# Optimization experiments

Measured on AMD Instinct MI355X. Metric: run time of the kernel, lower is better.

The kernel has to match this reference:

```python
import jax, jax.numpy as jnp
import numpy as np

NEG_SLOPE = 0.01  # F.leaky_relu default


def grid_sample_bilinear(im, pts):
    """torch.nn.functional.grid_sample equivalent, mode='bilinear',
    align_corners=True, padding_mode='zeros'.
    im: [B, C, H, W], pts: [B, N, 2] in [-1, 1] (x, y order). Returns [B, C, N].
    """
    B, C, H, W = im.shape
    x = (pts[..., 0] + 1.0) * 0.5 * (W - 1)  # [B, N]
    y = (pts[..., 1] + 1.0) * 0.5 * (H - 1)
    x0 = jnp.floor(x)
    y0 = jnp.floor(y)
    wx1 = x - x0
    wy1 = y - y0
    wx0 = 1.0 - wx1
    wy0 = 1.0 - wy1
    x0i = x0.astype(jnp.int32)
    y0i = y0.astype(jnp.int32)
    x1i = x0i + 1
    y1i = y0i + 1

    def corner(yi, xi, w):
        valid = (xi >= 0) & (xi < W) & (yi >= 0) & (yi < H)
        yc = jnp.clip(yi, 0, H - 1)
        xc = jnp.clip(xi, 0, W - 1)
        # gather per-batch: [B, C, N]
        g = jax.vmap(lambda f, yy, xx: f[:, yy, xx])(im, yc, xc)
        return g * (w * valid.astype(im.dtype))[:, None, :]

    return (corner(y0i, x0i, wy0 * wx0) + corner(y0i, x1i, wy0 * wx1)
            + corner(y1i, x0i, wy1 * wx0) + corner(y1i, x1i, wy1 * wx1))


def conv1x1(x, w, b):
    # x: [B, Cin, N], w: [Cout, Cin], b: [Cout] -> [B, Cout, N]
    return jnp.einsum('oi,bin->bon', w, x) + b[None, :, None]


def setup_inputs() -> dict:
    key = jax.random.key(0)
    ks = jax.random.split(key, 9)
    B, N, C, H, W = 64, 6890, 256, 56, 56
    filter_channels = [256, 128, 64, 5]
    points = jax.random.uniform(ks[0], (B, N, 2), jnp.float32, -1.0, 1.0)
    im_feat = jax.random.normal(ks[1], (B, C, H, W), jnp.float32)

    def mk_conv(k, cin, cout):
        k1, k2 = jax.random.split(k)
        bound = 1.0 / np.sqrt(cin)
        w = jax.random.uniform(k1, (cout, cin), jnp.float32, -bound, bound)
        b = jax.random.uniform(k2, (cout,), jnp.float32, -bound, bound)
        return w, b

    w0, b0 = mk_conv(ks[2], filter_channels[0], filter_channels[1])
    w1, b1 = mk_conv(ks[3], filter_channels[1] + filter_channels[0], filter_channels[2])
    w2, b2 = mk_conv(ks[4], filter_channels[2] + filter_channels[0], filter_channels[3])
    return {"points": points, "im_feat": im_feat,
            "w0": w0, "b0": b0, "w1": w1, "b1": b1, "w2": w2, "b2": b2}


def reference(points, im_feat, w0, b0, w1, b1, w2, b2):
    # sampling: bilinear gather of point-wise features, [B, C_s, N]
    point_feat = grid_sample_bilinear(im_feat, points)
    # reduce_dim: 1x1 conv MLP with skip-concat of the input features
    y = jax.nn.leaky_relu(conv1x1(point_feat, w0, b0), NEG_SLOPE)
    y = jax.nn.leaky_relu(conv1x1(jnp.concatenate([y, point_feat], axis=1), w1, b1), NEG_SLOPE)
    y = conv1x1(jnp.concatenate([y, point_feat], axis=1), w2, b2)  # last layer: no leaky_relu
    y = jax.nn.relu(y)  # self.last_op
    mesh_align_feat = y.reshape(y.shape[0], -1)  # [B, C_p * N]
    return (mesh_align_feat, point_feat)
```

## Files before the change

### kernel.cpp

```cpp
#include <hip/hip_runtime.h>

#define B_    64
#define C_    256
#define H_    56
#define W_    56
#define N_    6890
#define HW_   3136
#define NTILE 108

#define WB1_OFF (128*256)
#define WB2_OFF (128*256 + 64*384)
#define WTOT    (128*256 + 64*384 + 5*320)

typedef __attribute__((ext_vector_type(8))) __bf16 bf16x8;
typedef __attribute__((ext_vector_type(8))) unsigned short ushort8;
typedef __attribute__((ext_vector_type(4))) float f32x4;
typedef __attribute__((ext_vector_type(2))) float f32x2;
typedef __attribute__((ext_vector_type(4))) unsigned int uint4v;
typedef __attribute__((ext_vector_type(2))) unsigned int uint2v;

__device__ __forceinline__ unsigned short f2bf(float f) {
    unsigned int u = __builtin_bit_cast(unsigned int, f);
    u += 0x7FFFu + ((u >> 16) & 1u);
    return (unsigned short)(u >> 16);
}
__device__ __forceinline__ unsigned int pack2(float lo, float hi) {
    return (unsigned int)f2bf(lo) | ((unsigned int)f2bf(hi) << 16);
}
__device__ __forceinline__ float leaky(float v) { return v > 0.f ? v : 0.01f * v; }
__device__ __forceinline__ int pswz(int p) { return p ^ ((p >> 3) & 7); }

__global__ void wconv_kernel(const float* __restrict__ w0, const float* __restrict__ w1,
                             const float* __restrict__ w2, unsigned short* __restrict__ wb) {
    int i = blockIdx.x * 256 + threadIdx.x;
    if (i >= WTOT) return;
    float v = (i < WB1_OFF) ? w0[i] : (i < WB2_OFF) ? w1[i - WB1_OFF] : w2[i - WB2_OFF];
    wb[i] = f2bf(v);
}

__global__ __launch_bounds__(512, 6) void gather_kernel(
    const float* __restrict__ points, const float* __restrict__ im,
    float* __restrict__ out1) {
    __shared__ float Ls[HW_ * 4];

    const int t   = threadIdx.x;
    const int bid = blockIdx.x;
    const int b  = ((bid & 7) << 3) | ((bid >> 3) & 7);
    const int ch = bid >> 6;

    const f32x4* im4 = (const f32x4*)(im + ((size_t)b * C_ + ch * 4) * HW_);
#pragma unroll
    for (int g0 = 0; g0 < 2; g0++) {
        int g = t + (g0 << 9);
        if (g < 784) {
            f32x4 r0 = im4[g];
            f32x4 r1 = im4[784 + g];
            f32x4 r2 = im4[1568 + g];
            f32x4 r3 = im4[2352 + g];
#pragma unroll
            for (int i = 0; i < 4; i++) {
                f32x4 v; v[0] = r0[i]; v[1] = r1[i]; v[2] = r2[i]; v[3] = r3[i];
                *(f32x4*)(Ls + (pswz((g << 2) + i) << 2)) = v;
            }
        }
    }
    __syncthreads();

    const float* ptb = points + (size_t)b * N_ * 2;
    const size_t ob0 = ((size_t)b * C_ + ch * 4) * N_;
#pragma unroll 2
    for (int p = 0; p < 14; p++) {
        int n = t + (p << 9);
        if (n < N_) {
            f32x2 pt = *(const f32x2*)(ptb + 2 * n);
            float fx = fminf(fmaxf((pt.x + 1.f) * 27.5f, 0.f), 55.f);
            float fy = fminf(fmaxf((pt.y + 1.f) * 27.5f, 0.f), 55.f);
            float x0f = floorf(fx), y0f = floorf(fy);
            int x0 = (int)x0f, y0 = (int)y0f;
            float wx1 = fx - x0f, wy1 = fy - y0f;
            float wx0 = 1.f - wx1, wy0 = 1.f - wy1;
            bool hix = x0 >= W_ - 1;
            int   xb  = hix ? W_ - 2 : x0;
            float wxl = hix ? 0.f : wx0;
            float wxr = hix ? wx0 : wx1;
            int y0c = min(y0, H_ - 1);
            int y1c = min(y0 + 1, H_ - 1);
            float w00 = wy0 * wxl, w01 = wy0 * wxr;
            float w10 = wy1 * wxl, w11 = wy1 * wxr;
            int ia0 = y0c * W_ + xb, ia1 = y1c * W_ + xb;

            f32x4 q00 = *(const f32x4*)(Ls + (pswz(ia0)     << 2));
            f32x4 q01 = *(const f32x4*)(Ls + (pswz(ia0 + 1) << 2));
            f32x4 q10 = *(const f32x4*)(Ls + (pswz(ia1)     << 2));
            f32x4 q11 = *(const f32x4*)(Ls + (pswz(ia1 + 1) << 2));
            float v0 = w00*q00[0] + w01*q01[0] + w10*q10[0] + w11*q11[0];
            float v1 = w00*q00[1] + w01*q01[1] + w10*q10[1] + w11*q11[1];
            float v2 = w00*q00[2] + w01*q01[2] + w10*q10[2] + w11*q11[2];
            float v3 = w00*q00[3] + w01*q01[3] + w10*q10[3] + w11*q11[3];
            out1[ob0 + n]          = v0;
            out1[ob0 + N_ + n]     = v1;
            out1[ob0 + 2*N_ + n]   = v2;
            out1[ob0 + 3*N_ + n]   = v3;
        }
    }
}

__device__ __forceinline__ bf16x8 afrag_f32(const float* __restrict__ wp, int ldk,
                                            int rowbase, int k0, int lane, int nrows) {
    int i = rowbase + (lane & 15);
    int k = k0 + ((lane >> 4) << 3);
    ushort8 u;
    if (i < nrows) {
        const float* s = wp + (size_t)i * ldk + k;
#pragma unroll
        for (int j = 0; j < 8; j++) u[j] = f2bf(s[j]);
    } else {
#pragma unroll
        for (int j = 0; j < 8; j++) u[j] = 0;
    }
    return __builtin_bit_cast(bf16x8, u);
}
__device__ __forceinline__ bf16x8 afrag_bf(const unsigned short* __restrict__ wb, int ldk,
                                           int rowbase, int k0, int lane, int nrows) {
    int i = rowbase + (lane & 15);
    int k = k0 + ((lane >> 4) << 3);
    if (i < nrows) return __builtin_bit_cast(bf16x8, *(const ushort8*)(wb + (size_t)i * ldk + k));
    ushort8 z = {0, 0, 0, 0, 0, 0, 0, 0};
    return __builtin_bit_cast(bf16x8, z);
}

__device__ __forceinline__ bf16x8 bfrag(const unsigned int* buf, int rowstride_dw,
                                        int n, int k0) {
    int cd = (k0 >> 1) ^ ((n & 7) << 2);
    uint4v v = *(const uint4v*)(buf + n * rowstride_dw + cd);
    return __builtin_bit_cast(bf16x8, v);
}

template <bool BF16W>
__global__ __launch_bounds__(256) void mlp_kernel(
    const float* __restrict__ pf,
    const float* __restrict__ w0, const float* __restrict__ b0,
    const float* __restrict__ w1, const float* __restrict__ b1,
    const float* __restrict__ w2, const float* __restrict__ b2,
    const unsigned short* __restrict__ wb,
    float* __restrict__ out0) {
    __shared__ unsigned int Xs[64 * 128];
    __shared__ unsigned int Y0s[64 * 64];

    const int t    = threadIdx.x;
    const int lane = t & 63;
    const int wave = t >> 6;
    const int bid  = blockIdx.x;
    const int b    = bid / NTILE;
    const int tile = bid - b * NTILE;
    const int n0   = tile * 64;

    const int nn_g = min(n0 + lane, N_ - 1);
    const int swz  = (lane & 7) << 2;

    const float* pfb = pf + (size_t)b * C_ * N_;
#pragma unroll
    for (int g8 = 0; g8 < 8; g8++) {
        int c0 = wave * 64 + g8 * 8;
        float v[8];
#pragma unroll
        for (int j = 0; j < 8; j++) v[j] = pfb[(size_t)(c0 + j) * N_ + nn_g];
        uint4v pk;
        pk[0] = pack2(v[0], v[1]); pk[1] = pack2(v[2], v[3]);
        pk[2] = pack2(v[4], v[5]); pk[3] = pack2(v[6], v[7]);
        *(uint4v*)(Xs + lane * 128 + ((c0 >> 1) ^ swz)) = pk;
    }

    bf16x8 a1[2][8];
#pragma unroll
    for (int mt = 0; mt < 2; mt++)
#pragma unroll
        for (int ks = 0; ks < 8; ks++)
            a1[mt][ks] = BF16W ? afrag_bf(wb, 256, (wave * 2 + mt) * 16, ks * 32, lane, 1 << 30)
                               : afrag_f32(w0, 256, (wave * 2 + mt) * 16, ks * 32, lane, 1 << 30);

    __syncthreads();

    const int cl = lane & 15;
    const int rh = lane >> 4;
    const int kq = rh << 3;

    f32x4 acc1[2][4] = {};
#pragma unroll
    for (int ks = 0; ks < 8; ks++) {
        bf16x8 bx[4];
#pragma unroll
        for (int nt = 0; nt < 4; nt++)
            bx[nt] = bfrag(Xs, 128, nt * 16 + cl, ks * 32 + kq);
#pragma unroll
        for (int mt = 0; mt < 2; mt++)
#pragma unroll
            for (int nt = 0; nt < 4; nt++)
                acc1[mt][nt] = __builtin_amdgcn_mfma_f32_16x16x32_bf16(
                    a1[mt][ks], bx[nt], acc1[mt][nt], 0, 0, 0);
    }

#pragma unroll
    for (int mt = 0; mt < 2; mt++) {
        int m0 = (wave * 2 + mt) * 16 + (rh << 2);
        f32x4 bias = *(const f32x4*)(b0 + m0);
#pragma unroll
        for (int nt = 0; nt < 4; nt++) {
            int nn = nt * 16 + cl;
            float v0 = leaky(acc1[mt][nt][0] + bias[0]);
            float v1 = leaky(acc1[mt][nt][1] + bias[1]);
            float v2 = leaky(acc1[mt][nt][2] + bias[2]);
            float v3 = leaky(acc1[mt][nt][3] + bias[3]);
            int md = (m0 >> 1) ^ ((nn & 7) << 2);
            uint2v pk; pk[0] = pack2(v0, v1); pk[1] = pack2(v2, v3);
            *(uint2v*)(Y0s + nn * 64 + md) = pk;
        }
    }

    bf16x8 a2[12];
#pragma unroll
    for (int ks = 0; ks < 12; ks++)
        a2[ks] = BF16W ? afrag_bf(wb + WB1_OFF, 384, wave * 16, ks * 32, lane, 1 << 30)
                       : afrag_f32(w1, 384, wave * 16, ks * 32, lane, 1 << 30);

    __syncthreads();

    f32x4 acc2[4] = {};
#pragma unroll
    for (int ks = 0; ks < 12; ks++) {
#pragma unroll
        for (int nt = 0; nt < 4; nt++) {
            bf16x8 bx = (ks < 4) ? bfrag(Y0s, 64, nt * 16 + cl, ks * 32 + kq)
                                 : bfrag(Xs, 128, nt * 16 + cl, (ks - 4) * 32 + kq);
            acc2[nt] = __builtin_amdgcn_mfma_f32_16x16x32_bf16(a2[ks], bx, acc2[nt], 0, 0, 0);
        }
    }

    bf16x8 a3[10];
#pragma unroll
    for (int ks = 0; ks < 10; ks++)
        a3[ks] = BF16W ? afrag_bf(wb + WB2_OFF, 320, 0, ks * 32, lane, 5)
                       : afrag_f32(w2, 320, 0, ks * 32, lane, 5);

    __syncthreads();

    {
        int m0 = wave * 16 + (rh << 2);
        f32x4 bias = *(const f32x4*)(b1 + m0);
#pragma unroll
        for (int nt = 0; nt < 4; nt++) {
            int nn = nt * 16 + cl;
            float v0 = leaky(acc2[nt][0] + bias[0]);
            float v1 = leaky(acc2[nt][1] + bias[1]);
            float v2 = leaky(acc2[nt][2] + bias[2]);
            float v3 = leaky(acc2[nt][3] + bias[3]);
            int md = (m0 >> 1) ^ ((nn & 7) << 2);
            uint2v pk; pk[0] = pack2(v0, v1); pk[1] = pack2(v2, v3);
            *(uint2v*)(Y0s + nn * 32 + md) = pk;
        }
    }

    __syncthreads();

    {
        int nn = wave * 16 + cl;
        f32x4 acc3 = {};
#pragma unroll
        for (int ks = 0; ks < 10; ks++) {
            bf16x8 bx = (ks < 2) ? bfrag(Y0s, 32, nn, ks * 32 + kq)
                                 : bfrag(Xs, 128, nn, (ks - 2) * 32 + kq);
            acc3 = __builtin_amdgcn_mfma_f32_16x16x32_bf16(a3[ks], bx, acc3, 0, 0, 0);
        }
        int gn2 = n0 + nn;
        if (gn2 < N_) {
#pragma unroll
            for (int r = 0; r < 4; r++) {
                int m = (rh << 2) + r;
                if (m < 5) {
                    float v = acc3[r] + b2[m];
                    v = v > 0.f ? v : 0.f;
                    out0[((size_t)b * 5 + m) * N_ + gn2] = v;
                }
            }
        }
    }
}

extern "C" void kernel_launch(void* const* d_in, const int* in_sizes, int n_in,
                              void* d_out, int out_size, void* d_ws, size_t ws_size,
                              hipStream_t stream) {
    const float* points = (const float*)d_in[0];
    const float* im     = (const float*)d_in[1];
    const float* w0     = (const float*)d_in[2];
    const float* b0     = (const float*)d_in[3];
    const float* w1     = (const float*)d_in[4];
    const float* b1     = (const float*)d_in[5];
    const float* w2     = (const float*)d_in[6];
    const float* b2     = (const float*)d_in[7];
    float* out0 = (float*)d_out;
    float* out1 = out0 + (size_t)B_ * 5 * N_;

    const size_t WBYTES = (size_t)WTOT * 2;
    const bool wok = (d_ws != nullptr) && (ws_size >= WBYTES);
    unsigned short* wb = (unsigned short*)d_ws;

    if (wok) {
        hipLaunchKernelGGL(wconv_kernel, dim3((WTOT + 255) / 256), dim3(256), 0, stream,
                           w0, w1, w2, wb);
    }
    hipLaunchKernelGGL(gather_kernel, dim3(B_ * 64), dim3(512), 0, stream,
                       points, im, out1);
    if (wok) {
        hipLaunchKernelGGL(mlp_kernel<true>, dim3(B_ * NTILE), dim3(256), 0, stream,
                           out1, w0, b0, w1, b1, w2, b2, wb, out0);
    } else {
        hipLaunchKernelGGL(mlp_kernel<false>, dim3(B_ * NTILE), dim3(256), 0, stream,
                           out1, w0, b0, w1, b1, w2, b2, (const unsigned short*)nullptr, out0);
    }
}
```

Measured before the change: 318.2 us.

## Split gather and MLP into batch chunks for L2/MALL reuse of point features

Launches the gather and MLP kernels in two chunks of 32 batches each instead of one pass over all 64 batches. Batch indices are remapped so each XCD handles the same batches in both kernels, and the MLP visits batches in reverse order of the gather. The intent is that the point features the gather just wrote are still in the XCD-local L2 or the last-level cache when the MLP reads them, avoiding a full HBM round trip of the large intermediate. The cost is extra kernel launches and smaller grids per launch, which can leave tail gaps between kernels.

```diff
diff --git a/kernel.cpp b/kernel.cpp
--- a/kernel.cpp
+++ b/kernel.cpp
@@ -7,6 +7,7 @@
 #define N_    6890
 #define HW_   3136
 #define NTILE 108
+#define GB_   32
 
 #define WB1_OFF (128*256)
 #define WB2_OFF (128*256 + 64*384)
@@ -40,13 +41,15 @@
 
 __global__ __launch_bounds__(512, 6) void gather_kernel(
     const float* __restrict__ points, const float* __restrict__ im,
-    float* __restrict__ out1) {
+    float* __restrict__ out1, int b0) {
     __shared__ float Ls[HW_ * 4];
 
     const int t   = threadIdx.x;
     const int bid = blockIdx.x;
-    const int b  = ((bid & 7) << 3) | ((bid >> 3) & 7);
-    const int ch = bid >> 6;
+    const int xcd  = bid & 7;
+    const int ch   = (bid >> 3) & 63;
+    const int blow = bid >> 9;
+    const int b    = b0 + (blow << 3) + xcd;
 
     const f32x4* im4 = (const f32x4*)(im + ((size_t)b * C_ + ch * 4) * HW_);
 #pragma unroll
@@ -139,11 +142,11 @@
 template <bool BF16W>
 __global__ __launch_bounds__(256) void mlp_kernel(
     const float* __restrict__ pf,
-    const float* __restrict__ w0, const float* __restrict__ b0,
+    const float* __restrict__ w0, const float* __restrict__ b0_,
     const float* __restrict__ w1, const float* __restrict__ b1,
     const float* __restrict__ w2, const float* __restrict__ b2,
     const unsigned short* __restrict__ wb,
-    float* __restrict__ out0) {
+    float* __restrict__ out0, int b0) {
     __shared__ unsigned int Xs[64 * 128];
     __shared__ unsigned int Y0s[64 * 64];
 
@@ -151,9 +154,12 @@
     const int lane = t & 63;
     const int wave = t >> 6;
     const int bid  = blockIdx.x;
-    const int b    = bid / NTILE;
-    const int tile = bid - b * NTILE;
-    const int n0   = tile * 64;
+    const int xcd   = bid & 7;
+    const int r     = bid >> 3;
+    const int tile  = r % NTILE;
+    const int blowr = (GB_ / 8 - 1) - r / NTILE;
+    const int b     = b0 + (blowr << 3) + xcd;
+    const int n0    = tile * 64;
 
     const int nn_g = min(n0 + lane, N_ - 1);
     const int swz  = (lane & 7) << 2;
@@ -203,7 +209,7 @@
 #pragma unroll
     for (int mt = 0; mt < 2; mt++) {
         int m0 = (wave * 2 + mt) * 16 + (rh << 2);
-        f32x4 bias = *(const f32x4*)(b0 + m0);
+        f32x4 bias = *(const f32x4*)(b0_ + m0);
 #pragma unroll
         for (int nt = 0; nt < 4; nt++) {
             int nn = nt * 16 + cl;
@@ -274,10 +280,10 @@
         int gn2 = n0 + nn;
         if (gn2 < N_) {
 #pragma unroll
-            for (int r = 0; r < 4; r++) {
-                int m = (rh << 2) + r;
+            for (int r2 = 0; r2 < 4; r2++) {
+                int m = (rh << 2) + r2;
                 if (m < 5) {
-                    float v = acc3[r] + b2[m];
+                    float v = acc3[r2] + b2[m];
                     v = v > 0.f ? v : 0.f;
                     out0[((size_t)b * 5 + m) * N_ + gn2] = v;
                 }
@@ -308,13 +314,17 @@
         hipLaunchKernelGGL(wconv_kernel, dim3((WTOT + 255) / 256), dim3(256), 0, stream,
                            w0, w1, w2, wb);
     }
-    hipLaunchKernelGGL(gather_kernel, dim3(B_ * 64), dim3(512), 0, stream,
-                       points, im, out1);
-    if (wok) {
-        hipLaunchKernelGGL(mlp_kernel<true>, dim3(B_ * NTILE), dim3(256), 0, stream,
-                           out1, w0, b0, w1, b1, w2, b2, wb, out0);
-    } else {
-        hipLaunchKernelGGL(mlp_kernel<false>, dim3(B_ * NTILE), dim3(256), 0, stream,
-                           out1, w0, b0, w1, b1, w2, b2, (const unsigned short*)nullptr, out0);
-    }
-}
+    for (int g = 0; g < B_ / GB_; g++) {
+        const int bb = g * GB_;
+        hipLaunchKernelGGL(gather_kernel, dim3(GB_ * 64), dim3(512), 0, stream,
+                           points, im, out1, bb);
+        if (wok) {
+            hipLaunchKernelGGL(mlp_kernel<true>, dim3(GB_ * NTILE), dim3(256), 0, stream,
+                               out1, w0, b0, w1, b1, w2, b2, wb, out0, bb);
+        } else {
+            hipLaunchKernelGGL(mlp_kernel<false>, dim3(GB_ * NTILE), dim3(256), 0, stream,
+                               out1, w0, b0, w1, b1, w2, b2,
+                               (const unsigned short*)nullptr, out0, bb);
+        }
+    }
+}
```

Result: slower. 334.3 us (+5.1%).

## Transpose image to channels-last and fuse bilinear gather into MLP kernel

Applied to the files above, without the earlier changes.

Adds a transpose kernel that converts the image feature map to [B, HW, C] layout in workspace. A new fused kernel then gathers bilinear samples per point directly from global memory as contiguous channel vectors, writes point_feat, and runs the three-layer MFMA MLP from shared memory. This removes the re-read of the full point_feat tensor by the separate MLP kernel. In exchange it adds a full image transpose pass (about 200MB of traffic) and relies on cached global gathers instead of LDS-resident image tiles. It needs a large workspace and otherwise falls back to the old path.

```diff
diff --git a/kernel.cpp b/kernel.cpp
--- a/kernel.cpp
+++ b/kernel.cpp
@@ -38,34 +38,294 @@
     wb[i] = f2bf(v);
 }
 
+__global__ __launch_bounds__(256) void transpose_kernel(
+    const float* __restrict__ im, float* __restrict__ imT) {
+    __shared__ float Lt[64][68];
+    const int t   = threadIdx.x;
+    const int bid = blockIdx.x;
+    const int xcd  = bid & 7;
+    const int rest = bid >> 3;
+    const int b    = ((rest & 7) << 3) + xcd;
+    const int tl   = rest >> 3;
+    const int pt   = tl % 49, ct = tl / 49;
+    const int p0   = pt * 64, c0 = ct * 64;
+
+    const float* src = im + ((size_t)b * C_ + c0) * HW_ + p0;
+#pragma unroll
+    for (int rr = 0; rr < 4; rr++) {
+        int c_loc = (t >> 4) + rr * 16;
+        int pq    = (t & 15) << 2;
+        f32x4 v = *(const f32x4*)(src + (size_t)c_loc * HW_ + pq);
+        Lt[c_loc][pq]     = v[0];
+        Lt[c_loc][pq + 1] = v[1];
+        Lt[c_loc][pq + 2] = v[2];
+        Lt[c_loc][pq + 3] = v[3];
+    }
+    __syncthreads();
+    float* dst = imT + ((size_t)b * HW_ + p0) * C_ + c0;
+#pragma unroll
+    for (int i = 0; i < 4; i++) {
+        int idx = t + (i << 8);
+        int pr  = idx >> 4;
+        int c4  = (idx & 15) << 2;
+        f32x4 v;
+        v[0] = Lt[c4][pr]; v[1] = Lt[c4 + 1][pr];
+        v[2] = Lt[c4 + 2][pr]; v[3] = Lt[c4 + 3][pr];
+        *(f32x4*)(dst + (size_t)pr * C_ + c4) = v;
+    }
+}
+
+__device__ __forceinline__ bf16x8 bfrag(const unsigned int* buf, int rowstride_dw,
+                                        int n, int k0) {
+    int cd = (k0 >> 1) ^ ((n & 7) << 2);
+    uint4v v = *(const uint4v*)(buf + n * rowstride_dw + cd);
+    return __builtin_bit_cast(bf16x8, v);
+}
+__device__ __forceinline__ bf16x8 afrag_bf(const unsigned short* __restrict__ wb, int ldk,
+                                           int rowbase, int k0, int lane, int nrows) {
+    int i = rowbase + (lane & 15);
+    int k = k0 + ((lane >> 4) << 3);
+    if (i < nrows) return __builtin_bit_cast(bf16x8, *(const ushort8*)(wb + (size_t)i * ldk + k));
+    ushort8 z = {0, 0, 0, 0, 0, 0, 0, 0};
+    return __builtin_bit_cast(bf16x8, z);
+}
+
+__global__ __launch_bounds__(256, 2) void fused_kernel(
+    const float* __restrict__ points, const float* __restrict__ imT,
+    const float* __restrict__ b0_, const float* __restrict__ b1,
+    const float* __restrict__ b2, const unsigned short* __restrict__ wb,
+    float* __restrict__ out0, float* __restrict__ out1) {
+    __shared__ float Ls[16384];
+    __shared__ float Pw[64][4];
+    __shared__ int   Pi[64][2];
+
+    const int t    = threadIdx.x;
+    const int lane = t & 63;
+    const int wave = t >> 6;
+    const int bid  = blockIdx.x;
+    const int xcd  = bid & 7;
+    const int rr   = bid >> 3;
+    const int tile = rr % NTILE;
+    const int b    = (rr / NTILE) * 8 + xcd;
+    const int n0   = tile * 64;
+
+    if (t < 64) {
+        int n = min(n0 + t, N_ - 1);
+        f32x2 pt = *(const f32x2*)(points + ((size_t)b * N_ + n) * 2);
+        float fx = fminf(fmaxf((pt.x + 1.f) * 27.5f, 0.f), 55.f);
+        float fy = fminf(fmaxf((pt.y + 1.f) * 27.5f, 0.f), 55.f);
+        float x0f = floorf(fx), y0f = floorf(fy);
+        int x0 = (int)x0f, y0 = (int)y0f;
+        float wx1 = fx - x0f, wy1 = fy - y0f;
+        float wx0 = 1.f - wx1, wy0 = 1.f - wy1;
+        bool hix = x0 >= W_ - 1;
+        int   xb  = hix ? W_ - 2 : x0;
+        float wxl = hix ? 0.f : wx0;
+        float wxr = hix ? wx0 : wx1;
+        int y0c = min(y0, H_ - 1);
+        int y1c = min(y0 + 1, H_ - 1);
+        Pw[t][0] = wy0 * wxl; Pw[t][1] = wy0 * wxr;
+        Pw[t][2] = wy1 * wxl; Pw[t][3] = wy1 * wxr;
+        Pi[t][0] = y0c * W_ + xb; Pi[t][1] = y1c * W_ + xb;
+    }
+    __syncthreads();
+
+    const float* ib = imT + (size_t)b * HW_ * C_;
+#pragma unroll
+    for (int i = 0; i < 16; i += 2) {
+        int pA = wave * 16 + i, pB = pA + 1;
+        float wA0 = Pw[pA][0], wA1 = Pw[pA][1], wA2 = Pw[pA][2], wA3 = Pw[pA][3];
+        float wB0 = Pw[pB][0], wB1 = Pw[pB][1], wB2 = Pw[pB][2], wB3 = Pw[pB][3];
+        int aA0 = Pi[pA][0], aA1 = Pi[pA][1];
+        int aB0 = Pi[pB][0], aB1 = Pi[pB][1];
+        const float* sA0 = ib + ((size_t)aA0 << 8) + (lane << 2);
+        const float* sA1 = ib + ((size_t)aA1 << 8) + (lane << 2);
+        const float* sB0 = ib + ((size_t)aB0 << 8) + (lane << 2);
+        const float* sB1 = ib + ((size_t)aB1 << 8) + (lane << 2);
+        f32x4 cA00 = *(const f32x4*)(sA0);
+        f32x4 cA01 = *(const f32x4*)(sA0 + 256);
+        f32x4 cA10 = *(const f32x4*)(sA1);
+        f32x4 cA11 = *(const f32x4*)(sA1 + 256);
+        f32x4 cB00 = *(const f32x4*)(sB0);
+        f32x4 cB01 = *(const f32x4*)(sB0 + 256);
+        f32x4 cB10 = *(const f32x4*)(sB1);
+        f32x4 cB11 = *(const f32x4*)(sB1 + 256);
+        f32x4 vA, vB;
+#pragma unroll
+        for (int j = 0; j < 4; j++) {
+            vA[j] = wA0 * cA00[j] + wA1 * cA01[j] + wA2 * cA10[j] + wA3 * cA11[j];
+            vB[j] = wB0 * cB00[j] + wB1 * cB01[j] + wB2 * cB10[j] + wB3 * cB11[j];
+        }
+        *(f32x4*)(Ls + pA * 256 + ((lane ^ (pA & 7)) << 2)) = vA;
+        *(f32x4*)(Ls + pB * 256 + ((lane ^ (pB & 7)) << 2)) = vB;
+    }
+    __syncthreads();
+
+    f32x4 xr[16];
+#pragma unroll
+    for (int q = 0; q < 16; q++) {
+        int qd = (wave * 16 + q) ^ (lane & 7);
+        xr[q] = *(const f32x4*)(Ls + lane * 256 + (qd << 2));
+    }
+    __syncthreads();
+
+    unsigned int* Xs  = (unsigned int*)Ls;
+    unsigned int* Y0s = (unsigned int*)Ls + 8192;
+    {
+        float* pfb = out1 + (size_t)b * C_ * N_ + n0;
+        const bool okn = (n0 + lane) < N_;
+        const int swz = (lane & 7) << 2;
+#pragma unroll
+        for (int q = 0; q < 16; q += 2) {
+            int c0 = wave * 64 + q * 4;
+            if (okn) {
+#pragma unroll
+                for (int jj = 0; jj < 4; jj++) {
+                    pfb[(size_t)(c0 + jj) * N_ + lane]     = xr[q][jj];
+                    pfb[(size_t)(c0 + 4 + jj) * N_ + lane] = xr[q + 1][jj];
+                }
+            }
+            uint4v pk;
+            pk[0] = pack2(xr[q][0], xr[q][1]);     pk[1] = pack2(xr[q][2], xr[q][3]);
+            pk[2] = pack2(xr[q + 1][0], xr[q + 1][1]); pk[3] = pack2(xr[q + 1][2], xr[q + 1][3]);
+            *(uint4v*)(Xs + lane * 128 + ((c0 >> 1) ^ swz)) = pk;
+        }
+    }
+
+    bf16x8 a1[2][8];
+#pragma unroll
+    for (int mt = 0; mt < 2; mt++)
+#pragma unroll
+        for (int ks = 0; ks < 8; ks++)
+            a1[mt][ks] = afrag_bf(wb, 256, (wave * 2 + mt) * 16, ks * 32, lane, 1 << 30);
+
+    __syncthreads();
+
+    const int cl = lane & 15;
+    const int rh = lane >> 4;
+    const int kq = rh << 3;
+
+    f32x4 acc1[2][4] = {};
+#pragma unroll
+    for (int ks = 0; ks < 8; ks++) {
+        bf16x8 bx[4];
+#pragma unroll
+        for (int nt = 0; nt < 4; nt++)
+            bx[nt] = bfrag(Xs, 128, nt * 16 + cl, ks * 32 + kq);
+#pragma unroll
+        for (int mt = 0; mt < 2; mt++)
+#pragma unroll
+            for (int nt = 0; nt < 4; nt++)
+                acc1[mt][nt] = __builtin_amdgcn_mfma_f32_16x16x32_bf16(
+                    a1[mt][ks], bx[nt], acc1[mt][nt], 0, 0, 0);
+    }
+
+#pragma unroll
+    for (int mt = 0; mt < 2; mt++) {
+        int m0 = (wave * 2 + mt) * 16 + (rh << 2);
+        f32x4 bias = *(const f32x4*)(b0_ + m0);
+#pragma unroll
+        for (int nt = 0; nt < 4; nt++) {
+            int nn = nt * 16 + cl;
+            float v0 = leaky(acc1[mt][nt][0] + bias[0]);
+            float v1 = leaky(acc1[mt][nt][1] + bias[1]);
+            float v2 = leaky(acc1[mt][nt][2] + bias[2]);
+            float v3 = leaky(acc1[mt][nt][3] + bias[3]);
+            int md = (m0 >> 1) ^ ((nn & 7) << 2);
+            uint2v pk; pk[0] = pack2(v0, v1); pk[1] = pack2(v2, v3);
+            *(uint2v*)(Y0s + nn * 64 + md) = pk;
+        }
+    }
+
+    bf16x8 a2[12];
+#pragma unroll
+    for (int ks = 0; ks < 12; ks++)
+        a2[ks] = afrag_bf(wb + WB1_OFF, 384, wave * 16, ks * 32, lane, 1 << 30);
+
+    __syncthreads();
+
+    f32x4 acc2[4] = {};
+#pragma unroll
+    for (int ks = 0; ks < 12; ks++) {
+#pragma unroll
+        for (int nt = 0; nt < 4; nt++) {
+            bf16x8 bx = (ks < 4) ? bfrag(Y0s, 64, nt * 16 + cl, ks * 32 + kq)
+                                 : bfrag(Xs, 128, nt * 16 + cl, (ks - 4) * 32 + kq);
+            acc2[nt] = __builtin_amdgcn_mfma_f32_16x16x32_bf16(a2[ks], bx, acc2[nt], 0, 0, 0);
+        }
+    }
+
+    bf16x8 a3[10];
+#pragma unroll
+    for (int ks = 0; ks < 10; ks++)
+        a3[ks] = afrag_bf(wb + WB2_OFF, 320, 0, ks * 32, lane, 5);
+
+    __syncthreads();
+
+    {
+        int m0 = wave * 16 + (rh << 2);
+        f32x4 bias = *(const f32x4*)(b1 + m0);
+#pragma unroll
+        for (int nt = 0; nt < 4; nt++) {
+            int nn = nt * 16 + cl;
+            float v0 = leaky(acc2[nt][0] + bias[0]);
+            float v1 = leaky(acc2[nt][1] + bias[1]);
+            float v2 = leaky(acc2[nt][2] + bias[2]);
+            float v3 = leaky(acc2[nt][3] + bias[3]);
+            int md = (m0 >> 1) ^ ((nn & 7) << 2);
+            uint2v pk; pk[0] = pack2(v0, v1); pk[1] = pack2(v2, v3);
+            *(uint2v*)(Y0s + nn * 32 + md) = pk;
+        }
+    }
+
+    __syncthreads();
+
+    {
+        int nn = wave * 16 + cl;
+        f32x4 acc3 = {};
+#pragma unroll
+        for (int ks = 0; ks < 10; ks++) {
+            bf16x8 bx = (ks < 2) ? bfrag(Y0s, 32, nn, ks * 32 + kq)
+                                 : bfrag(Xs, 128, nn, (ks - 2) * 32 + kq);
+            acc3 = __builtin_amdgcn_mfma_f32_16x16x32_bf16(a3[ks], bx, acc3, 0, 0, 0);
+        }
+        int gn2 = n0 + nn;
+        if (gn2 < N_) {
+#pragma unroll
+            for (int r2 = 0; r2 < 4; r2++) {
+                int m = (rh << 2) + r2;
+                if (m < 5) {
+                    float v = acc3[r2] + b2[m];
+                    v = v > 0.f ? v : 0.f;
+                    out0[((size_t)b * 5 + m) * N_ + gn2] = v;
+                }
+            }
+        }
+    }
+}
+
 __global__ __launch_bounds__(512, 6) void gather_kernel(
     const float* __restrict__ points, const float* __restrict__ im,
     float* __restrict__ out1) {
-    __shared__ float Ls[HW_ * 4];
-
+    __shared__ float Lg[HW_ * 4];
     const int t   = threadIdx.x;
     const int bid = blockIdx.x;
     const int b  = ((bid & 7) << 3) | ((bid >> 3) & 7);
     const int ch = bid >> 6;
-
     const f32x4* im4 = (const f32x4*)(im + ((size_t)b * C_ + ch * 4) * HW_);
 #pragma unroll
     for (int g0 = 0; g0 < 2; g0++) {
         int g = t + (g0 << 9);
         if (g < 784) {
-            f32x4 r0 = im4[g];
-            f32x4 r1 = im4[784 + g];
-            f32x4 r2 = im4[1568 + g];
-            f32x4 r3 = im4[2352 + g];
+            f32x4 r0 = im4[g], r1 = im4[784 + g], r2 = im4[1568 + g], r3 = im4[2352 + g];
 #pragma unroll
             for (int i = 0; i < 4; i++) {
                 f32x4 v; v[0] = r0[i]; v[1] = r1[i]; v[2] = r2[i]; v[3] = r3[i];
-                *(f32x4*)(Ls + (pswz((g << 2) + i) << 2)) = v;
+                *(f32x4*)(Lg + (pswz((g << 2) + i) << 2)) = v;
             }
         }
     }
     __syncthreads();
-
     const float* ptb = points + (size_t)b * N_ * 2;
     const size_t ob0 = ((size_t)b * C_ + ch * 4) * N_;
 #pragma unroll 2
@@ -85,22 +345,16 @@
             float wxr = hix ? wx0 : wx1;
             int y0c = min(y0, H_ - 1);
             int y1c = min(y0 + 1, H_ - 1);
-            float w00 = wy0 * wxl, w01 = wy0 * wxr;
-            float w10 = wy1 * wxl, w11 = wy1 * wxr;
+            float w00 = wy0 * wxl, w01 = wy0 * wxr, w10 = wy1 * wxl, w11 = wy1 * wxr;
             int ia0 = y0c * W_ + xb, ia1 = y1c * W_ + xb;
-
-            f32x4 q00 = *(const f32x4*)(Ls + (pswz(ia0)     << 2));
-            f32x4 q01 = *(const f32x4*)(Ls + (pswz(ia0 + 1) << 2));
-            f32x4 q10 = *(const f32x4*)(Ls + (pswz(ia1)     << 2));
-            f32x4 q11 = *(const f32x4*)(Ls + (pswz(ia1 + 1) << 2));
-            float v0 = w00*q00[0] + w01*q01[0] + w10*q10[0] + w11*q11[0];
-            float v1 = w00*q00[1] + w01*q01[1] + w10*q10[1] + w11*q11[1];
-            float v2 = w00*q00[2] + w01*q01[2] + w10*q10[2] + w11*q11[2];
-            float v3 = w00*q00[3] + w01*q01[3] + w10*q10[3] + w11*q11[3];
-            out1[ob0 + n]          = v0;
-            out1[ob0 + N_ + n]     = v1;
-            out1[ob0 + 2*N_ + n]   = v2;
-            out1[ob0 + 3*N_ + n]   = v3;
+            f32x4 q00 = *(const f32x4*)(Lg + (pswz(ia0)     << 2));
+            f32x4 q01 = *(const f32x4*)(Lg + (pswz(ia0 + 1) << 2));
+            f32x4 q10 = *(const f32x4*)(Lg + (pswz(ia1)     << 2));
+            f32x4 q11 = *(const f32x4*)(Lg + (pswz(ia1 + 1) << 2));
+            out1[ob0 + n]        = w00*q00[0] + w01*q01[0] + w10*q10[0] + w11*q11[0];
+            out1[ob0 + N_ + n]   = w00*q00[1] + w01*q01[1] + w10*q10[1] + w11*q11[1];
+            out1[ob0 + 2*N_ + n] = w00*q00[2] + w01*q01[2] + w10*q10[2] + w11*q11[2];
+            out1[ob0 + 3*N_ + n] = w00*q00[3] + w01*q01[3] + w10*q10[3] + w11*q11[3];
         }
     }
 }
@@ -120,33 +374,17 @@
     }
     return __builtin_bit_cast(bf16x8, u);
 }
-__device__ __forceinline__ bf16x8 afrag_bf(const unsigned short* __restrict__ wb, int ldk,
-                                           int rowbase, int k0, int lane, int nrows) {
-    int i = rowbase + (lane & 15);
-    int k = k0 + ((lane >> 4) << 3);
-    if (i < nrows) return __builtin_bit_cast(bf16x8, *(const ushort8*)(wb + (size_t)i * ldk + k));
-    ushort8 z = {0, 0, 0, 0, 0, 0, 0, 0};
-    return __builtin_bit_cast(bf16x8, z);
-}
-
-__device__ __forceinline__ bf16x8 bfrag(const unsigned int* buf, int rowstride_dw,
-                                        int n, int k0) {
-    int cd = (k0 >> 1) ^ ((n & 7) << 2);
-    uint4v v = *(const uint4v*)(buf + n * rowstride_dw + cd);
-    return __builtin_bit_cast(bf16x8, v);
-}
 
 template <bool BF16W>
 __global__ __launch_bounds__(256) void mlp_kernel(
     const float* __restrict__ pf,
-    const float* __restrict__ w0, const float* __restrict__ b0,
+    const float* __restrict__ w0, const float* __restrict__ b0_,
     const float* __restrict__ w1, const float* __restrict__ b1,
     const float* __restrict__ w2, const float* __restrict__ b2,
     const unsigned short* __restrict__ wb,
     float* __restrict__ out0) {
     __shared__ unsigned int Xs[64 * 128];
     __shared__ unsigned int Y0s[64 * 64];
-
     const int t    = threadIdx.x;
     const int lane = t & 63;
     const int wave = t >> 6;
@@ -154,10 +392,8 @@
     const int b    = bid / NTILE;
     const int tile = bid - b * NTILE;
     const int n0   = tile * 64;
-
     const int nn_g = min(n0 + lane, N_ - 1);
     const int swz  = (lane & 7) << 2;
-
     const float* pfb = pf + (size_t)b * C_ * N_;
 #pragma unroll
     for (int g8 = 0; g8 < 8; g8++) {
@@ -170,7 +406,6 @@
         pk[2] = pack2(v[4], v[5]); pk[3] = pack2(v[6], v[7]);
         *(uint4v*)(Xs + lane * 128 + ((c0 >> 1) ^ swz)) = pk;
     }
-
     bf16x8 a1[2][8];
 #pragma unroll
     for (int mt = 0; mt < 2; mt++)
@@ -178,13 +413,10 @@
         for (int ks = 0; ks < 8; ks++)
             a1[mt][ks] = BF16W ? afrag_bf(wb, 256, (wave * 2 + mt) * 16, ks * 32, lane, 1 << 30)
                                : afrag_f32(w0, 256, (wave * 2 + mt) * 16, ks * 32, lane, 1 << 30);
-
-    __syncthreads();
-
+    __syncthreads();
     const int cl = lane & 15;
     const int rh = lane >> 4;
     const int kq = rh << 3;
-
     f32x4 acc1[2][4] = {};
 #pragma unroll
     for (int ks = 0; ks < 8; ks++) {
@@ -199,11 +431,10 @@
                 acc1[mt][nt] = __builtin_amdgcn_mfma_f32_16x16x32_bf16(
                     a1[mt][ks], bx[nt], acc1[mt][nt], 0, 0, 0);
     }
-
 #pragma unroll
     for (int mt = 0; mt < 2; mt++) {
         int m0 = (wave * 2 + mt) * 16 + (rh << 2);
-        f32x4 bias = *(const f32x4*)(b0 + m0);
+        f32x4 bias = *(const f32x4*)(b0_ + m0);
 #pragma unroll
         for (int nt = 0; nt < 4; nt++) {
             int nn = nt * 16 + cl;
@@ -216,15 +447,12 @@
             *(uint2v*)(Y0s + nn * 64 + md) = pk;
         }
     }
-
     bf16x8 a2[12];
 #pragma unroll
     for (int ks = 0; ks < 12; ks++)
         a2[ks] = BF16W ? afrag_bf(wb + WB1_OFF, 384, wave * 16, ks * 32, lane, 1 << 30)
                        : afrag_f32(w1, 384, wave * 16, ks * 32, lane, 1 << 30);
-
-    __syncthreads();
-
+    __syncthreads();
     f32x4 acc2[4] = {};
 #pragma unroll
     for (int ks = 0; ks < 12; ks++) {
@@ -235,15 +463,12 @@
             acc2[nt] = __builtin_amdgcn_mfma_f32_16x16x32_bf16(a2[ks], bx, acc2[nt], 0, 0, 0);
         }
     }
-
     bf16x8 a3[10];
 #pragma unroll
     for (int ks = 0; ks < 10; ks++)
         a3[ks] = BF16W ? afrag_bf(wb + WB2_OFF, 320, 0, ks * 32, lane, 5)
                        : afrag_f32(w2, 320, 0, ks * 32, lane, 5);
-
-    __syncthreads();
-
+    __syncthreads();
     {
         int m0 = wave * 16 + (rh << 2);
         f32x4 bias = *(const f32x4*)(b1 + m0);
@@ -259,9 +484,7 @@
             *(uint2v*)(Y0s + nn * 32 + md) = pk;
         }
     }
-
-    __syncthreads();
-
+    __syncthreads();
     {
         int nn = wave * 16 + cl;
         f32x4 acc3 = {};
@@ -274,10 +497,10 @@
         int gn2 = n0 + nn;
         if (gn2 < N_) {
 #pragma unroll
-            for (int r = 0; r < 4; r++) {
-                int m = (rh << 2) + r;
+            for (int r2 = 0; r2 < 4; r2++) {
+                int m = (rh << 2) + r2;
                 if (m < 5) {
-                    float v = acc3[r] + b2[m];
+                    float v = acc3[r2] + b2[m];
                     v = v > 0.f ? v : 0.f;
                     out0[((size_t)b * 5 + m) * N_ + gn2] = v;
                 }
@@ -300,21 +523,32 @@
     float* out0 = (float*)d_out;
     float* out1 = out0 + (size_t)B_ * 5 * N_;
 
+    const size_t TBYTES = (size_t)B_ * HW_ * C_ * 4;
     const size_t WBYTES = (size_t)WTOT * 2;
-    const bool wok = (d_ws != nullptr) && (ws_size >= WBYTES);
-    unsigned short* wb = (unsigned short*)d_ws;
+    const bool fok = (d_ws != nullptr) && (ws_size >= TBYTES + WBYTES);
+    const bool wok = fok || ((d_ws != nullptr) && (ws_size >= WBYTES));
+    float*          imT = (float*)d_ws;
+    unsigned short* wb  = fok ? (unsigned short*)((char*)d_ws + TBYTES)
+                              : (unsigned short*)d_ws;
 
     if (wok) {
         hipLaunchKernelGGL(wconv_kernel, dim3((WTOT + 255) / 256), dim3(256), 0, stream,
                            w0, w1, w2, wb);
     }
-    hipLaunchKernelGGL(gather_kernel, dim3(B_ * 64), dim3(512), 0, stream,
-                       points, im, out1);
-    if (wok) {
-        hipLaunchKernelGGL(mlp_kernel<true>, dim3(B_ * NTILE), dim3(256), 0, stream,
-                           out1, w0, b0, w1, b1, w2, b2, wb, out0);
+    if (fok) {
+        hipLaunchKernelGGL(transpose_kernel, dim3(B_ * 196), dim3(256), 0, stream, im, imT);
+        hipLaunchKernelGGL(fused_kernel, dim3(B_ * NTILE), dim3(256), 0, stream,
+                           points, imT, b0, b1, b2, wb, out0, out1);
     } else {
-        hipLaunchKernelGGL(mlp_kernel<false>, dim3(B_ * NTILE), dim3(256), 0, stream,
-                           out1, w0, b0, w1, b1, w2, b2, (const unsigned short*)nullptr, out0);
-    }
-}
+        hipLaunchKernelGGL(gather_kernel, dim3(B_ * 64), dim3(512), 0, stream,
+                           points, im, out1);
+        if (wok) {
+            hipLaunchKernelGGL(mlp_kernel<true>, dim3(B_ * NTILE), dim3(256), 0, stream,
+                               out1, w0, b0, w1, b1, w2, b2, wb, out0);
+        } else {
+            hipLaunchKernelGGL(mlp_kernel<false>, dim3(B_ * NTILE), dim3(256), 0, stream,
+                               out1, w0, b0, w1, b1, w2, b2,
+                               (const unsigned short*)nullptr, out0);
+        }
+    }
+}
```

Result: slower. 393.0 us (+23.5%).
